# Kernel tuning notes

Hardware: AMD Instinct MI355X
Metric: run time of the kernel (lower is better)

## Reference

```python
import jax, jax.numpy as jnp
import numpy as np


def setup_inputs() -> dict:
    key = jax.random.key(0)
    k1, k2 = jax.random.split(key)
    inputs = jax.random.normal(k1, (64, 32, 32, 64), dtype=jnp.float32)
    # codebook param: (embedding_dim=64, n_embedding=1024), variance-scaling uniform fan_in
    fan_in = 64
    limit = float(np.sqrt(3.0 / fan_in))
    embeddings = jax.random.uniform(k2, (64, 1024), dtype=jnp.float32,
                                    minval=-limit, maxval=limit)
    return {"inputs": inputs, "embeddings": embeddings}


def reference(inputs, embeddings):
    commitment_cost = 0.25
    D, K = embeddings.shape  # (embedding_dim, n_embedding)
    flat = inputs.reshape(-1, D)  # [N, D]
    distances = (jnp.sum(jnp.square(flat), 1, keepdims=True)
                 - 2.0 * jnp.matmul(flat, embeddings)
                 + jnp.sum(jnp.square(embeddings), 0, keepdims=True))
    encoding_indices_flat = jnp.argmax(-distances, 1)  # [N]
    encodings = jax.nn.one_hot(encoding_indices_flat, K, dtype=distances.dtype)  # [N, K]
    encoding_indices = encoding_indices_flat.reshape(inputs.shape[:-1])  # [B,H,W]
    quantized = embeddings.T[encoding_indices]  # gather -> [B,H,W,D]

    e_latent_loss = jnp.mean(jnp.square(jax.lax.stop_gradient(quantized) - inputs))
    q_latent_loss = jnp.mean(jnp.square(quantized - jax.lax.stop_gradient(inputs)))
    loss = q_latent_loss + commitment_cost * e_latent_loss

    # straight-through estimator
    quantized_st = inputs + jax.lax.stop_gradient(quantized - inputs)

    avg_probs = jnp.mean(encodings, 0)
    perplexity = jnp.exp(-jnp.sum(avg_probs * jnp.log(avg_probs + 1e-10)))
    return (quantized_st, loss, perplexity, encodings, encoding_indices, distances)
```

## Files before the change

kernel.cpp:

```cpp
#include <hip/hip_runtime.h>
#include <math.h>

#define NROWS   65536
#define DIMS    64
#define KCODES  1024

static constexpr size_t QST_OFF  = 0;
static constexpr size_t LOSS_OFF = 4194304;
static constexpr size_t PERP_OFF = 4194305;
static constexpr size_t ENC_OFF  = 4194306;
static constexpr size_t IDX_OFF  = 71303170;
static constexpr size_t DIST_OFF = 71368706;

#define XSTRIDE 132

__global__ void enorm_kernel(const float* __restrict__ emb, float* __restrict__ enorm) {
    #pragma clang fp contract(off)
    int k = blockIdx.x * blockDim.x + threadIdx.x;
    float s = 0.f;
    for (int d = 0; d < DIMS; ++d) {
        float e  = emb[(size_t)d * KCODES + k];
        float sq = e * e;
        s = s + sq;
    }
    enorm[k] = s;
}

__global__ __launch_bounds__(512, 4) void vq_dist(
    const float* __restrict__ x, const float* __restrict__ emb,
    const float* __restrict__ enorm, float* __restrict__ out,
    unsigned long long* __restrict__ winners)
{
    #pragma clang fp contract(off)
    __shared__ __align__(16) float xs_t[32 * XSTRIDE];
    __shared__ __align__(16) float es_t[32 * XSTRIDE];
    __shared__ float xnl[128];

    const int tid = threadIdx.x;
    const int tc  = tid & 15;
    const int tr  = tid >> 4;
    const int kt  = blockIdx.x & 7;
    const int br  = blockIdx.x >> 3;
    const size_t n0 = (size_t)br * 128;

    const float* xg = x + n0 * DIMS;
    const float* eg = emb + kt * 128;

    float acc[4][8];
    #pragma unroll
    for (int j = 0; j < 4; ++j)
        #pragma unroll
        for (int jj = 0; jj < 8; ++jj) acc[j][jj] = 0.f;

    float rr[8];

    for (int h = 0; h < 2; ++h) {
        __syncthreads();
        #pragma unroll
        for (int i = 0; i < 2; ++i) {
            int c = tid + 512 * i;
            int row = c >> 3, dq = c & 7;
            float4 v = *(const float4*)(xg + (size_t)row * DIMS + h * 32 + dq * 4);
            xs_t[(dq * 4 + 0) * XSTRIDE + row] = v.x;
            xs_t[(dq * 4 + 1) * XSTRIDE + row] = v.y;
            xs_t[(dq * 4 + 2) * XSTRIDE + row] = v.z;
            xs_t[(dq * 4 + 3) * XSTRIDE + row] = v.w;
        }
        #pragma unroll
        for (int i = 0; i < 2; ++i) {
            int c = tid + 512 * i;
            int d2 = c >> 5, kq = c & 31;
            float4 v = *(const float4*)(eg + (size_t)(h * 32 + d2) * KCODES + kq * 4);
            es_t[d2 * XSTRIDE + kq * 4 + 0] = v.x;
            es_t[d2 * XSTRIDE + kq * 4 + 1] = v.y;
            es_t[d2 * XSTRIDE + kq * 4 + 2] = v.z;
            es_t[d2 * XSTRIDE + kq * 4 + 3] = v.w;
        }
        __syncthreads();

        if (tid < 128) {
            if (h == 0) {
                #pragma unroll
                for (int j = 0; j < 8; ++j) { float v = xs_t[j * XSTRIDE + tid]; rr[j] = v * v; }
                for (int i = 8; i < 32; i += 8)
                    #pragma unroll
                    for (int j = 0; j < 8; ++j) { float v = xs_t[(i + j) * XSTRIDE + tid]; float sq = v * v; rr[j] = rr[j] + sq; }
            } else {
                for (int i = 0; i < 32; i += 8)
                    #pragma unroll
                    for (int j = 0; j < 8; ++j) { float v = xs_t[(i + j) * XSTRIDE + tid]; float sq = v * v; rr[j] = rr[j] + sq; }
                xnl[tid] = ((rr[0] + rr[1]) + (rr[2] + rr[3])) + ((rr[4] + rr[5]) + (rr[6] + rr[7]));
            }
        }

        #pragma unroll 4
        for (int d2 = 0; d2 < 32; ++d2) {
            float4 xr = *(const float4*)&xs_t[d2 * XSTRIDE + tr * 4];
            float4 ea = *(const float4*)&es_t[d2 * XSTRIDE + tc * 4];
            float4 eb = *(const float4*)&es_t[d2 * XSTRIDE + 64 + tc * 4];
            float xv[4] = {xr.x, xr.y, xr.z, xr.w};
            #pragma unroll
            for (int j = 0; j < 4; ++j) {
                acc[j][0] = fmaf(xv[j], ea.x, acc[j][0]);
                acc[j][1] = fmaf(xv[j], ea.y, acc[j][1]);
                acc[j][2] = fmaf(xv[j], ea.z, acc[j][2]);
                acc[j][3] = fmaf(xv[j], ea.w, acc[j][3]);
                acc[j][4] = fmaf(xv[j], eb.x, acc[j][4]);
                acc[j][5] = fmaf(xv[j], eb.y, acc[j][5]);
                acc[j][6] = fmaf(xv[j], eb.z, acc[j][6]);
                acc[j][7] = fmaf(xv[j], eb.w, acc[j][7]);
            }
        }
    }
    __syncthreads();

    const float4 en0 = *(const float4*)(enorm + kt * 128 + tc * 4);
    const float4 en1 = *(const float4*)(enorm + kt * 128 + 64 + tc * 4);
    const float4 z4 = make_float4(0.f, 0.f, 0.f, 0.f);

    #pragma unroll
    for (int j = 0; j < 4; ++j) {
        const int row = tr * 4 + j;
        const float xnr = xnl[row];
        float4 da, db;
        { float m = 2.0f * acc[j][0]; float t = xnr - m; da.x = t + en0.x; }
        { float m = 2.0f * acc[j][1]; float t = xnr - m; da.y = t + en0.y; }
        { float m = 2.0f * acc[j][2]; float t = xnr - m; da.z = t + en0.z; }
        { float m = 2.0f * acc[j][3]; float t = xnr - m; da.w = t + en0.w; }
        { float m = 2.0f * acc[j][4]; float t = xnr - m; db.x = t + en1.x; }
        { float m = 2.0f * acc[j][5]; float t = xnr - m; db.y = t + en1.y; }
        { float m = 2.0f * acc[j][6]; float t = xnr - m; db.z = t + en1.z; }
        { float m = 2.0f * acc[j][7]; float t = xnr - m; db.w = t + en1.w; }

        const size_t rowg = n0 + row;
        float* dr = out + DIST_OFF + rowg * (size_t)KCODES + kt * 128 + tc * 4;
        *(float4*)dr = da; *(float4*)(dr + 64) = db;
        float* er = out + ENC_OFF + rowg * (size_t)KCODES + kt * 128 + tc * 4;
        *(float4*)er = z4; *(float4*)(er + 64) = z4;

        float bv = da.x; int kloc = tc * 4;
        if (da.y < bv) { bv = da.y; kloc = tc * 4 + 1; }
        if (da.z < bv) { bv = da.z; kloc = tc * 4 + 2; }
        if (da.w < bv) { bv = da.w; kloc = tc * 4 + 3; }
        if (db.x < bv) { bv = db.x; kloc = 64 + tc * 4; }
        if (db.y < bv) { bv = db.y; kloc = 64 + tc * 4 + 1; }
        if (db.z < bv) { bv = db.z; kloc = 64 + tc * 4 + 2; }
        if (db.w < bv) { bv = db.w; kloc = 64 + tc * 4 + 3; }

        int ib = __float_as_int(bv);
        unsigned mk = (unsigned)ib ^ ((unsigned)(ib >> 31) | 0x80000000u);
        unsigned long long key = ((unsigned long long)mk << 32) | (unsigned)(kt * 128 + kloc);

        #pragma unroll
        for (int m = 1; m < 16; m <<= 1) {
            unsigned long long ok = __shfl_xor(key, m);
            if (ok < key) key = ok;
        }
        if (tc == 0) atomicMin(&winners[rowg], key);
    }
}

__global__ __launch_bounds__(256) void vq_finish(
    const float* __restrict__ x, const float* __restrict__ emb,
    const unsigned long long* __restrict__ winners, float* __restrict__ out,
    float* __restrict__ counts, float* __restrict__ sqsum)
{
    __shared__ float bsum[4];
    const int tid = threadIdx.x;
    const size_t row = (size_t)blockIdx.x * 16 + (tid >> 4);
    const int q = tid & 15;
    const int k = (int)(winners[row] & 1023u);

    float4 e4;
    e4.x = emb[(size_t)(q * 4 + 0) * KCODES + k];
    e4.y = emb[(size_t)(q * 4 + 1) * KCODES + k];
    e4.z = emb[(size_t)(q * 4 + 2) * KCODES + k];
    e4.w = emb[(size_t)(q * 4 + 3) * KCODES + k];
    float4 x4 = *(const float4*)(x + row * DIMS + q * 4);
    *(float4*)(out + QST_OFF + row * DIMS + q * 4) = e4;

    float f0 = e4.x - x4.x, f1 = e4.y - x4.y, f2 = e4.z - x4.z, f3 = e4.w - x4.w;
    float ls = f0 * f0 + f1 * f1 + f2 * f2 + f3 * f3;
    #pragma unroll
    for (int m = 1; m < 64; m <<= 1) ls += __shfl_xor(ls, m);
    if ((tid & 63) == 0) bsum[tid >> 6] = ls;

    if (q == 0) {
        out[IDX_OFF + row] = (float)k;
        atomicAdd(&counts[k], 1.0f);
        out[ENC_OFF + row * (size_t)KCODES + k] = 1.0f;
    }
    __syncthreads();
    if (tid == 0) atomicAdd(sqsum, (bsum[0] + bsum[1]) + (bsum[2] + bsum[3]));
}

__global__ void vq_final(const float* __restrict__ counts, const float* __restrict__ sqsum,
                         float* __restrict__ out) {
    __shared__ double part[16];
    int tid = threadIdx.x;
    double p = (double)counts[tid] * (1.0 / 65536.0);
    double t = p * log(p + 1e-10);
    #pragma unroll
    for (int m = 1; m < 64; m <<= 1) t += __shfl_xor(t, m);
    if ((tid & 63) == 0) part[tid >> 6] = t;
    __syncthreads();
    if (tid == 0) {
        double s = 0.0;
        #pragma unroll
        for (int i = 0; i < 16; ++i) s += part[i];
        out[LOSS_OFF] = (float)(1.25 * (double)sqsum[0] * (1.0 / 4194304.0));
        out[PERP_OFF] = (float)exp(-s);
    }
}

extern "C" void kernel_launch(void* const* d_in, const int* in_sizes, int n_in,
                              void* d_out, int out_size, void* d_ws, size_t ws_size,
                              hipStream_t stream) {
    const float* x   = (const float*)d_in[0];
    const float* emb = (const float*)d_in[1];
    float* out = (float*)d_out;
    float* enorm  = (float*)d_ws;
    float* counts = enorm + KCODES;
    float* sqsum  = counts + KCODES;
    unsigned long long* winners = (unsigned long long*)((float*)d_ws + 4096);

    hipMemsetAsync(counts, 0, (KCODES + 1) * sizeof(float), stream);
    hipMemsetAsync(winners, 0xFF, NROWS * sizeof(unsigned long long), stream);
    enorm_kernel<<<KCODES / 256, 256, 0, stream>>>(emb, enorm);
    vq_dist<<<(NROWS / 128) * (KCODES / 128), 512, 0, stream>>>(x, emb, enorm, out, winners);
    vq_finish<<<NROWS / 16, 256, 0, stream>>>(x, emb, winners, out, counts, sqsum);
    vq_final<<<1, KCODES, 0, stream>>>(counts, sqsum, out);
}
```

Measured before the change: 264.8 us.

## Fuse distance, argmin and finish into one row-block kernel with double-buffered codebook

Each block now handles 128 rows against all 1024 codes, looping over code tiles with double-buffered shared-memory codebook slices and prefetching. The per-row argmin is kept in registers, which removes the global winners buffer, its memset and the 64-bit atomicMin. The quantized gather and loss are done in the same kernel using a transposed codebook built in the prep kernel. The trade-off is a much smaller grid and larger shared-memory footprint, which lowers parallelism for the store-heavy output writes.

```diff
diff --git a/kernel.cpp b/kernel.cpp
--- a/kernel.cpp
+++ b/kernel.cpp
@@ -4,6 +4,7 @@
 #define NROWS   65536
 #define DIMS    64
 #define KCODES  1024
+#define XL      132
 
 static constexpr size_t QST_OFF  = 0;
 static constexpr size_t LOSS_OFF = 4194304;
@@ -12,92 +13,98 @@
 static constexpr size_t IDX_OFF  = 71303170;
 static constexpr size_t DIST_OFF = 71368706;
 
-#define XSTRIDE 132
-
-__global__ void enorm_kernel(const float* __restrict__ emb, float* __restrict__ enorm) {
+__global__ void prep_kernel(const float* __restrict__ emb, float* __restrict__ enorm,
+                            float* __restrict__ embT) {
     #pragma clang fp contract(off)
     int k = blockIdx.x * blockDim.x + threadIdx.x;
     float s = 0.f;
     for (int d = 0; d < DIMS; ++d) {
-        float e  = emb[(size_t)d * KCODES + k];
+        float e = emb[(size_t)d * KCODES + k];
+        embT[(size_t)k * DIMS + d] = e;
         float sq = e * e;
         s = s + sq;
     }
     enorm[k] = s;
 }
 
-__global__ __launch_bounds__(512, 4) void vq_dist(
+__global__ __launch_bounds__(512, 4) void vq_fused(
     const float* __restrict__ x, const float* __restrict__ emb,
-    const float* __restrict__ enorm, float* __restrict__ out,
-    unsigned long long* __restrict__ winners)
+    const float* __restrict__ enorm, const float* __restrict__ embT,
+    float* __restrict__ out, float* __restrict__ counts, float* __restrict__ sqsum)
 {
     #pragma clang fp contract(off)
-    __shared__ __align__(16) float xs_t[32 * XSTRIDE];
-    __shared__ __align__(16) float es_t[32 * XSTRIDE];
-    __shared__ float xnl[128];
+    __shared__ __align__(16) float xs[DIMS * XL];
+    __shared__ __align__(16) float es[2][32 * XL];
+    __shared__ float xn[128];
+    __shared__ int   winner[128];
+    __shared__ float bsum[8];
 
     const int tid = threadIdx.x;
     const int tc  = tid & 15;
     const int tr  = tid >> 4;
-    const int kt  = blockIdx.x & 7;
-    const int br  = blockIdx.x >> 3;
-    const size_t n0 = (size_t)br * 128;
-
+    const size_t n0 = (size_t)blockIdx.x * 128;
     const float* xg = x + n0 * DIMS;
-    const float* eg = emb + kt * 128;
+
+    #pragma unroll
+    for (int i = 0; i < 4; ++i) {
+        int c = tid + 512 * i;
+        int row = c & 127, dq = c >> 7;
+        float4 v = *(const float4*)(xg + (size_t)row * DIMS + dq * 4);
+        xs[(dq * 4 + 0) * XL + row] = v.x;
+        xs[(dq * 4 + 1) * XL + row] = v.y;
+        xs[(dq * 4 + 2) * XL + row] = v.z;
+        xs[(dq * 4 + 3) * XL + row] = v.w;
+    }
+    {
+        int c0 = tid, c1 = tid + 512;
+        float4 a = *(const float4*)(emb + (size_t)(c0 >> 5) * KCODES + (c0 & 31) * 4);
+        float4 b = *(const float4*)(emb + (size_t)(c1 >> 5) * KCODES + (c1 & 31) * 4);
+        __syncthreads();
+        *(float4*)&es[0][(c0 >> 5) * XL + (c0 & 31) * 4] = a;
+        *(float4*)&es[0][(c1 >> 5) * XL + (c1 & 31) * 4] = b;
+    }
+    if (tid < 128) {
+        float rr[8];
+        #pragma unroll
+        for (int j = 0; j < 8; ++j) { float v = xs[j * XL + tid]; rr[j] = v * v; }
+        for (int i = 8; i < 64; i += 8)
+            #pragma unroll
+            for (int j = 0; j < 8; ++j) { float v = xs[(i + j) * XL + tid]; float sq = v * v; rr[j] = rr[j] + sq; }
+        xn[tid] = ((rr[0] + rr[1]) + (rr[2] + rr[3])) + ((rr[4] + rr[5]) + (rr[6] + rr[7]));
+    }
+    __syncthreads();
 
     float acc[4][8];
-    #pragma unroll
-    for (int j = 0; j < 4; ++j)
-        #pragma unroll
-        for (int jj = 0; jj < 8; ++jj) acc[j][jj] = 0.f;
-
-    float rr[8];
-
-    for (int h = 0; h < 2; ++h) {
-        __syncthreads();
-        #pragma unroll
-        for (int i = 0; i < 2; ++i) {
-            int c = tid + 512 * i;
-            int row = c >> 3, dq = c & 7;
-            float4 v = *(const float4*)(xg + (size_t)row * DIMS + h * 32 + dq * 4);
-            xs_t[(dq * 4 + 0) * XSTRIDE + row] = v.x;
-            xs_t[(dq * 4 + 1) * XSTRIDE + row] = v.y;
-            xs_t[(dq * 4 + 2) * XSTRIDE + row] = v.z;
-            xs_t[(dq * 4 + 3) * XSTRIDE + row] = v.w;
-        }
-        #pragma unroll
-        for (int i = 0; i < 2; ++i) {
-            int c = tid + 512 * i;
-            int d2 = c >> 5, kq = c & 31;
-            float4 v = *(const float4*)(eg + (size_t)(h * 32 + d2) * KCODES + kq * 4);
-            es_t[d2 * XSTRIDE + kq * 4 + 0] = v.x;
-            es_t[d2 * XSTRIDE + kq * 4 + 1] = v.y;
-            es_t[d2 * XSTRIDE + kq * 4 + 2] = v.z;
-            es_t[d2 * XSTRIDE + kq * 4 + 3] = v.w;
-        }
-        __syncthreads();
-
-        if (tid < 128) {
-            if (h == 0) {
+    float bv[4]; int bi[4];
+    #pragma unroll
+    for (int j = 0; j < 4; ++j) { bv[j] = 3.4e38f; bi[j] = 0; }
+    float4 en0, en1;
+    const float4 z4 = make_float4(0.f, 0.f, 0.f, 0.f);
+
+    for (int s = 0; s < 16; ++s) {
+        const int kt = s >> 1, h = s & 1, buf = s & 1;
+        if (h == 0) {
+            #pragma unroll
+            for (int j = 0; j < 4; ++j)
                 #pragma unroll
-                for (int j = 0; j < 8; ++j) { float v = xs_t[j * XSTRIDE + tid]; rr[j] = v * v; }
-                for (int i = 8; i < 32; i += 8)
-                    #pragma unroll
-                    for (int j = 0; j < 8; ++j) { float v = xs_t[(i + j) * XSTRIDE + tid]; float sq = v * v; rr[j] = rr[j] + sq; }
-            } else {
-                for (int i = 0; i < 32; i += 8)
-                    #pragma unroll
-                    for (int j = 0; j < 8; ++j) { float v = xs_t[(i + j) * XSTRIDE + tid]; float sq = v * v; rr[j] = rr[j] + sq; }
-                xnl[tid] = ((rr[0] + rr[1]) + (rr[2] + rr[3])) + ((rr[4] + rr[5]) + (rr[6] + rr[7]));
-            }
-        }
-
+                for (int m = 0; m < 8; ++m) acc[j][m] = 0.f;
+            en0 = *(const float4*)(enorm + kt * 128 + tc * 4);
+            en1 = *(const float4*)(enorm + kt * 128 + 64 + tc * 4);
+        }
+        float4 nt0, nt1;
+        if (s < 15) {
+            int sn = s + 1, ktn = sn >> 1, hn = sn & 1;
+            int c0 = tid, c1 = tid + 512;
+            nt0 = *(const float4*)(emb + (size_t)(hn * 32 + (c0 >> 5)) * KCODES + ktn * 128 + (c0 & 31) * 4);
+            nt1 = *(const float4*)(emb + (size_t)(hn * 32 + (c1 >> 5)) * KCODES + ktn * 128 + (c1 & 31) * 4);
+        }
+        const float* ep = es[buf];
+        const int dbase = h * 32;
         #pragma unroll 4
         for (int d2 = 0; d2 < 32; ++d2) {
-            float4 xr = *(const float4*)&xs_t[d2 * XSTRIDE + tr * 4];
-            float4 ea = *(const float4*)&es_t[d2 * XSTRIDE + tc * 4];
-            float4 eb = *(const float4*)&es_t[d2 * XSTRIDE + 64 + tc * 4];
+            float4 xr = *(const float4*)&xs[(dbase + d2) * XL + tr * 4];
+            float4 ea = *(const float4*)&ep[d2 * XL + tc * 4];
+            float4 eb = *(const float4*)&ep[d2 * XL + 64 + tc * 4];
             float xv[4] = {xr.x, xr.y, xr.z, xr.w};
             #pragma unroll
             for (int j = 0; j < 4; ++j) {
@@ -111,87 +118,98 @@
                 acc[j][7] = fmaf(xv[j], eb.w, acc[j][7]);
             }
         }
-    }
-    __syncthreads();
-
-    const float4 en0 = *(const float4*)(enorm + kt * 128 + tc * 4);
-    const float4 en1 = *(const float4*)(enorm + kt * 128 + 64 + tc * 4);
-    const float4 z4 = make_float4(0.f, 0.f, 0.f, 0.f);
+        if (h == 1) {
+            #pragma unroll
+            for (int j = 0; j < 4; ++j) {
+                const int row = tr * 4 + j;
+                const float xnr = xn[row];
+                float4 da, db;
+                { float m = 2.0f * acc[j][0]; float t = xnr - m; da.x = t + en0.x; }
+                { float m = 2.0f * acc[j][1]; float t = xnr - m; da.y = t + en0.y; }
+                { float m = 2.0f * acc[j][2]; float t = xnr - m; da.z = t + en0.z; }
+                { float m = 2.0f * acc[j][3]; float t = xnr - m; da.w = t + en0.w; }
+                { float m = 2.0f * acc[j][4]; float t = xnr - m; db.x = t + en1.x; }
+                { float m = 2.0f * acc[j][5]; float t = xnr - m; db.y = t + en1.y; }
+                { float m = 2.0f * acc[j][6]; float t = xnr - m; db.z = t + en1.z; }
+                { float m = 2.0f * acc[j][7]; float t = xnr - m; db.w = t + en1.w; }
+                const size_t rowg = n0 + row;
+                float* dr = out + DIST_OFF + rowg * (size_t)KCODES + kt * 128 + tc * 4;
+                *(float4*)dr = da; *(float4*)(dr + 64) = db;
+                float* er = out + ENC_OFF + rowg * (size_t)KCODES + kt * 128 + tc * 4;
+                *(float4*)er = z4; *(float4*)(er + 64) = z4;
+
+                float lv = da.x; int li = kt * 128 + tc * 4;
+                if (da.y < lv) { lv = da.y; li = kt * 128 + tc * 4 + 1; }
+                if (da.z < lv) { lv = da.z; li = kt * 128 + tc * 4 + 2; }
+                if (da.w < lv) { lv = da.w; li = kt * 128 + tc * 4 + 3; }
+                if (db.x < lv) { lv = db.x; li = kt * 128 + 64 + tc * 4; }
+                if (db.y < lv) { lv = db.y; li = kt * 128 + 64 + tc * 4 + 1; }
+                if (db.z < lv) { lv = db.z; li = kt * 128 + 64 + tc * 4 + 2; }
+                if (db.w < lv) { lv = db.w; li = kt * 128 + 64 + tc * 4 + 3; }
+                if (lv < bv[j]) { bv[j] = lv; bi[j] = li; }
+            }
+        }
+        if (s < 15) {
+            int bufn = (s + 1) & 1;
+            int c0 = tid, c1 = tid + 512;
+            *(float4*)&es[bufn][(c0 >> 5) * XL + (c0 & 31) * 4] = nt0;
+            *(float4*)&es[bufn][(c1 >> 5) * XL + (c1 & 31) * 4] = nt1;
+        }
+        asm volatile("s_waitcnt lgkmcnt(0)" ::: "memory");
+        __builtin_amdgcn_s_barrier();
+    }
+
+    __syncthreads();
 
     #pragma unroll
     for (int j = 0; j < 4; ++j) {
         const int row = tr * 4 + j;
-        const float xnr = xnl[row];
-        float4 da, db;
-        { float m = 2.0f * acc[j][0]; float t = xnr - m; da.x = t + en0.x; }
-        { float m = 2.0f * acc[j][1]; float t = xnr - m; da.y = t + en0.y; }
-        { float m = 2.0f * acc[j][2]; float t = xnr - m; da.z = t + en0.z; }
-        { float m = 2.0f * acc[j][3]; float t = xnr - m; da.w = t + en0.w; }
-        { float m = 2.0f * acc[j][4]; float t = xnr - m; db.x = t + en1.x; }
-        { float m = 2.0f * acc[j][5]; float t = xnr - m; db.y = t + en1.y; }
-        { float m = 2.0f * acc[j][6]; float t = xnr - m; db.z = t + en1.z; }
-        { float m = 2.0f * acc[j][7]; float t = xnr - m; db.w = t + en1.w; }
-
-        const size_t rowg = n0 + row;
-        float* dr = out + DIST_OFF + rowg * (size_t)KCODES + kt * 128 + tc * 4;
-        *(float4*)dr = da; *(float4*)(dr + 64) = db;
-        float* er = out + ENC_OFF + rowg * (size_t)KCODES + kt * 128 + tc * 4;
-        *(float4*)er = z4; *(float4*)(er + 64) = z4;
-
-        float bv = da.x; int kloc = tc * 4;
-        if (da.y < bv) { bv = da.y; kloc = tc * 4 + 1; }
-        if (da.z < bv) { bv = da.z; kloc = tc * 4 + 2; }
-        if (da.w < bv) { bv = da.w; kloc = tc * 4 + 3; }
-        if (db.x < bv) { bv = db.x; kloc = 64 + tc * 4; }
-        if (db.y < bv) { bv = db.y; kloc = 64 + tc * 4 + 1; }
-        if (db.z < bv) { bv = db.z; kloc = 64 + tc * 4 + 2; }
-        if (db.w < bv) { bv = db.w; kloc = 64 + tc * 4 + 3; }
-
-        int ib = __float_as_int(bv);
+        int ib = __float_as_int(bv[j]);
         unsigned mk = (unsigned)ib ^ ((unsigned)(ib >> 31) | 0x80000000u);
-        unsigned long long key = ((unsigned long long)mk << 32) | (unsigned)(kt * 128 + kloc);
-
+        unsigned long long key = ((unsigned long long)mk << 32) | (unsigned)bi[j];
         #pragma unroll
         for (int m = 1; m < 16; m <<= 1) {
             unsigned long long ok = __shfl_xor(key, m);
             if (ok < key) key = ok;
         }
-        if (tc == 0) atomicMin(&winners[rowg], key);
-    }
-}
-
-__global__ __launch_bounds__(256) void vq_finish(
-    const float* __restrict__ x, const float* __restrict__ emb,
-    const unsigned long long* __restrict__ winners, float* __restrict__ out,
-    float* __restrict__ counts, float* __restrict__ sqsum)
-{
-    __shared__ float bsum[4];
-    const int tid = threadIdx.x;
-    const size_t row = (size_t)blockIdx.x * 16 + (tid >> 4);
-    const int q = tid & 15;
-    const int k = (int)(winners[row] & 1023u);
-
-    float4 e4;
-    e4.x = emb[(size_t)(q * 4 + 0) * KCODES + k];
-    e4.y = emb[(size_t)(q * 4 + 1) * KCODES + k];
-    e4.z = emb[(size_t)(q * 4 + 2) * KCODES + k];
-    e4.w = emb[(size_t)(q * 4 + 3) * KCODES + k];
-    float4 x4 = *(const float4*)(x + row * DIMS + q * 4);
-    *(float4*)(out + QST_OFF + row * DIMS + q * 4) = e4;
-
-    float f0 = e4.x - x4.x, f1 = e4.y - x4.y, f2 = e4.z - x4.z, f3 = e4.w - x4.w;
-    float ls = f0 * f0 + f1 * f1 + f2 * f2 + f3 * f3;
-    #pragma unroll
-    for (int m = 1; m < 64; m <<= 1) ls += __shfl_xor(ls, m);
-    if ((tid & 63) == 0) bsum[tid >> 6] = ls;
-
-    if (q == 0) {
-        out[IDX_OFF + row] = (float)k;
-        atomicAdd(&counts[k], 1.0f);
-        out[ENC_OFF + row * (size_t)KCODES + k] = 1.0f;
-    }
-    __syncthreads();
-    if (tid == 0) atomicAdd(sqsum, (bsum[0] + bsum[1]) + (bsum[2] + bsum[3]));
+        if (tc == 0) {
+            int k = (int)(key & 1023u);
+            winner[row] = k;
+            out[IDX_OFF + n0 + row] = (float)k;
+            atomicAdd(&counts[k], 1.0f);
+            out[ENC_OFF + (n0 + row) * (size_t)KCODES + k] = 1.0f;
+        }
+    }
+    __syncthreads();
+
+    {
+        const int row = tid >> 2;
+        const int q4  = tid & 3;
+        const int k   = winner[row];
+        const float* et = embT + (size_t)k * DIMS + q4 * 16;
+        float* qo = out + QST_OFF + (n0 + row) * (size_t)DIMS + q4 * 16;
+        float ls = 0.f;
+        #pragma unroll
+        for (int i = 0; i < 4; ++i) {
+            float4 q = *(const float4*)(et + 4 * i);
+            *(float4*)(qo + 4 * i) = q;
+            float f0 = q.x - xs[(q4 * 16 + 4 * i + 0) * XL + row];
+            float f1 = q.y - xs[(q4 * 16 + 4 * i + 1) * XL + row];
+            float f2 = q.z - xs[(q4 * 16 + 4 * i + 2) * XL + row];
+            float f3 = q.w - xs[(q4 * 16 + 4 * i + 3) * XL + row];
+            ls += f0 * f0 + f1 * f1 + f2 * f2 + f3 * f3;
+        }
+        #pragma unroll
+        for (int m = 1; m < 64; m <<= 1) ls += __shfl_xor(ls, m);
+        if ((tid & 63) == 0) bsum[tid >> 6] = ls;
+    }
+    __syncthreads();
+    if (tid == 0) {
+        float s = 0.f;
+        #pragma unroll
+        for (int i = 0; i < 8; ++i) s += bsum[i];
+        atomicAdd(sqsum, s);
+    }
 }
 
 __global__ void vq_final(const float* __restrict__ counts, const float* __restrict__ sqsum,
@@ -222,12 +240,10 @@
     float* enorm  = (float*)d_ws;
     float* counts = enorm + KCODES;
     float* sqsum  = counts + KCODES;
-    unsigned long long* winners = (unsigned long long*)((float*)d_ws + 4096);
+    float* embT   = (float*)d_ws + 4096;
 
     hipMemsetAsync(counts, 0, (KCODES + 1) * sizeof(float), stream);
-    hipMemsetAsync(winners, 0xFF, NROWS * sizeof(unsigned long long), stream);
-    enorm_kernel<<<KCODES / 256, 256, 0, stream>>>(emb, enorm);
-    vq_dist<<<(NROWS / 128) * (KCODES / 128), 512, 0, stream>>>(x, emb, enorm, out, winners);
-    vq_finish<<<NROWS / 16, 256, 0, stream>>>(x, emb, winners, out, counts, sqsum);
+    prep_kernel<<<KCODES / 256, 256, 0, stream>>>(emb, enorm, embT);
+    vq_fused<<<NROWS / 128, 512, 0, stream>>>(x, emb, enorm, embT, out, counts, sqsum);
     vq_final<<<1, KCODES, 0, stream>>>(counts, sqsum, out);
 }
```

Result: no change. 266.6 us (+0.7%).

## Restructure distance kernel: load x tile once, loop over codebook tiles, nontemporal stores

Applied to the files above, without the earlier changes.

Each block of the distance kernel now loads its 128-row x tile into shared memory once and loops over four 128-code tiles, covering half the codebook. Previously eight blocks each reloaded the same x rows. Each thread computes an 8x8 output tile, reading embeddings straight from global memory with register prefetch instead of staging them in LDS. It keeps a running per-row argmin across tiles, so only one shuffle reduction and atomic happens per row. Distance, one-hot and quantized outputs use nontemporal 8-byte or 16-byte stores to limit cache pollution. In exchange, higher register pressure (64 accumulators) lowers occupancy, and the global stores are narrower than before.

```diff
diff --git a/kernel.cpp b/kernel.cpp
--- a/kernel.cpp
+++ b/kernel.cpp
@@ -4,6 +4,10 @@
 #define NROWS   65536
 #define DIMS    64
 #define KCODES  1024
+#define XL      132
+
+typedef float f32x2 __attribute__((ext_vector_type(2)));
+typedef float f32x4 __attribute__((ext_vector_type(4)));
 
 static constexpr size_t QST_OFF  = 0;
 static constexpr size_t LOSS_OFF = 4194304;
@@ -11,8 +15,6 @@
 static constexpr size_t ENC_OFF  = 4194306;
 static constexpr size_t IDX_OFF  = 71303170;
 static constexpr size_t DIST_OFF = 71368706;
-
-#define XSTRIDE 132
 
 __global__ void enorm_kernel(const float* __restrict__ emb, float* __restrict__ enorm) {
     #pragma clang fp contract(off)
@@ -26,137 +28,133 @@
     enorm[k] = s;
 }
 
-__global__ __launch_bounds__(512, 4) void vq_dist(
+__global__ __launch_bounds__(256, 3) void vq_dist(
     const float* __restrict__ x, const float* __restrict__ emb,
     const float* __restrict__ enorm, float* __restrict__ out,
     unsigned long long* __restrict__ winners)
 {
     #pragma clang fp contract(off)
-    __shared__ __align__(16) float xs_t[32 * XSTRIDE];
-    __shared__ __align__(16) float es_t[32 * XSTRIDE];
-    __shared__ float xnl[128];
+    __shared__ __align__(16) float xs[DIMS * XL];
+    __shared__ float xn[128];
 
     const int tid = threadIdx.x;
     const int tc  = tid & 15;
     const int tr  = tid >> 4;
-    const int kt  = blockIdx.x & 7;
-    const int br  = blockIdx.x >> 3;
-    const size_t n0 = (size_t)br * 128;
-
+    const int kb  = blockIdx.x & 1;
+    const int rb  = blockIdx.x >> 1;
+    const size_t n0 = (size_t)rb * 128;
     const float* xg = x + n0 * DIMS;
-    const float* eg = emb + kt * 128;
-
-    float acc[4][8];
-    #pragma unroll
-    for (int j = 0; j < 4; ++j)
-        #pragma unroll
-        for (int jj = 0; jj < 8; ++jj) acc[j][jj] = 0.f;
-
-    float rr[8];
-
-    for (int h = 0; h < 2; ++h) {
-        __syncthreads();
-        #pragma unroll
-        for (int i = 0; i < 2; ++i) {
-            int c = tid + 512 * i;
-            int row = c >> 3, dq = c & 7;
-            float4 v = *(const float4*)(xg + (size_t)row * DIMS + h * 32 + dq * 4);
-            xs_t[(dq * 4 + 0) * XSTRIDE + row] = v.x;
-            xs_t[(dq * 4 + 1) * XSTRIDE + row] = v.y;
-            xs_t[(dq * 4 + 2) * XSTRIDE + row] = v.z;
-            xs_t[(dq * 4 + 3) * XSTRIDE + row] = v.w;
+
+    #pragma unroll
+    for (int i = 0; i < 8; ++i) {
+        int c = i * 256 + tid;
+        int row = c >> 4, q = c & 15;
+        float4 v = *(const float4*)(xg + (size_t)row * DIMS + q * 4);
+        xs[(q * 4 + 0) * XL + row] = v.x;
+        xs[(q * 4 + 1) * XL + row] = v.y;
+        xs[(q * 4 + 2) * XL + row] = v.z;
+        xs[(q * 4 + 3) * XL + row] = v.w;
+    }
+    __syncthreads();
+    if (tid < 128) {
+        float rr[8];
+        #pragma unroll
+        for (int j = 0; j < 8; ++j) { float v = xs[j * XL + tid]; rr[j] = v * v; }
+        for (int i = 8; i < 64; i += 8)
+            #pragma unroll
+            for (int j = 0; j < 8; ++j) { float v = xs[(i + j) * XL + tid]; float sq = v * v; rr[j] = rr[j] + sq; }
+        xn[tid] = ((rr[0] + rr[1]) + (rr[2] + rr[3])) + ((rr[4] + rr[5]) + (rr[6] + rr[7]));
+    }
+    __syncthreads();
+
+    float bv[8]; int bi[8];
+    #pragma unroll
+    for (int j = 0; j < 8; ++j) { bv[j] = 3.4e38f; bi[j] = 0; }
+
+    for (int kt = 0; kt < 4; ++kt) {
+        const int kbase = kb * 512 + kt * 128 + tc * 8;
+        float acc[8][8];
+        #pragma unroll
+        for (int j = 0; j < 8; ++j)
+            #pragma unroll
+            for (int m = 0; m < 8; ++m) acc[j][m] = 0.f;
+
+        const float* ebase = emb + kbase;
+        float4 eA = *(const float4*)(ebase);
+        float4 eB = *(const float4*)(ebase + 4);
+        #pragma unroll 4
+        for (int d = 0; d < DIMS; ++d) {
+            float4 eAn, eBn;
+            if (d < DIMS - 1) {
+                const float* ep = ebase + (size_t)(d + 1) * KCODES;
+                eAn = *(const float4*)(ep);
+                eBn = *(const float4*)(ep + 4);
+            }
+            float4 x0 = *(const float4*)&xs[d * XL + tr * 8];
+            float4 x1 = *(const float4*)&xs[d * XL + tr * 8 + 4];
+            const float xv[8] = {x0.x, x0.y, x0.z, x0.w, x1.x, x1.y, x1.z, x1.w};
+            #pragma unroll
+            for (int j = 0; j < 8; ++j) {
+                acc[j][0] = fmaf(xv[j], eA.x, acc[j][0]);
+                acc[j][1] = fmaf(xv[j], eA.y, acc[j][1]);
+                acc[j][2] = fmaf(xv[j], eA.z, acc[j][2]);
+                acc[j][3] = fmaf(xv[j], eA.w, acc[j][3]);
+                acc[j][4] = fmaf(xv[j], eB.x, acc[j][4]);
+                acc[j][5] = fmaf(xv[j], eB.y, acc[j][5]);
+                acc[j][6] = fmaf(xv[j], eB.z, acc[j][6]);
+                acc[j][7] = fmaf(xv[j], eB.w, acc[j][7]);
+            }
+            eA = eAn; eB = eBn;
         }
-        #pragma unroll
-        for (int i = 0; i < 2; ++i) {
-            int c = tid + 512 * i;
-            int d2 = c >> 5, kq = c & 31;
-            float4 v = *(const float4*)(eg + (size_t)(h * 32 + d2) * KCODES + kq * 4);
-            es_t[d2 * XSTRIDE + kq * 4 + 0] = v.x;
-            es_t[d2 * XSTRIDE + kq * 4 + 1] = v.y;
-            es_t[d2 * XSTRIDE + kq * 4 + 2] = v.z;
-            es_t[d2 * XSTRIDE + kq * 4 + 3] = v.w;
+
+        const float4 enA = *(const float4*)(enorm + kbase);
+        const float4 enB = *(const float4*)(enorm + kbase + 4);
+        const float en[8] = {enA.x, enA.y, enA.z, enA.w, enB.x, enB.y, enB.z, enB.w};
+
+        #pragma unroll
+        for (int j = 0; j < 8; ++j) {
+            const int row = tr * 8 + j;
+            const float xnr = xn[row];
+            float dv[8];
+            #pragma unroll
+            for (int m = 0; m < 8; ++m) {
+                float mm = 2.0f * acc[j][m];
+                float tt = xnr - mm;
+                dv[m] = tt + en[m];
+            }
+            const size_t rowg = n0 + row;
+            float* dr = out + DIST_OFF + rowg * (size_t)KCODES + kbase;
+            f32x2 v01 = {dv[0], dv[1]}, v23 = {dv[2], dv[3]};
+            f32x2 v45 = {dv[4], dv[5]}, v67 = {dv[6], dv[7]};
+            __builtin_nontemporal_store(v01, (f32x2*)(dr));
+            __builtin_nontemporal_store(v23, (f32x2*)(dr + 2));
+            __builtin_nontemporal_store(v45, (f32x2*)(dr + 4));
+            __builtin_nontemporal_store(v67, (f32x2*)(dr + 6));
+            float* er = out + ENC_OFF + rowg * (size_t)KCODES + kbase;
+            const f32x2 z2 = {0.f, 0.f};
+            __builtin_nontemporal_store(z2, (f32x2*)(er));
+            __builtin_nontemporal_store(z2, (f32x2*)(er + 2));
+            __builtin_nontemporal_store(z2, (f32x2*)(er + 4));
+            __builtin_nontemporal_store(z2, (f32x2*)(er + 6));
+
+            float lv = dv[0]; int li = kbase;
+            #pragma unroll
+            for (int m = 1; m < 8; ++m) if (dv[m] < lv) { lv = dv[m]; li = kbase + m; }
+            if (lv < bv[j]) { bv[j] = lv; bi[j] = li; }
         }
-        __syncthreads();
-
-        if (tid < 128) {
-            if (h == 0) {
-                #pragma unroll
-                for (int j = 0; j < 8; ++j) { float v = xs_t[j * XSTRIDE + tid]; rr[j] = v * v; }
-                for (int i = 8; i < 32; i += 8)
-                    #pragma unroll
-                    for (int j = 0; j < 8; ++j) { float v = xs_t[(i + j) * XSTRIDE + tid]; float sq = v * v; rr[j] = rr[j] + sq; }
-            } else {
-                for (int i = 0; i < 32; i += 8)
-                    #pragma unroll
-                    for (int j = 0; j < 8; ++j) { float v = xs_t[(i + j) * XSTRIDE + tid]; float sq = v * v; rr[j] = rr[j] + sq; }
-                xnl[tid] = ((rr[0] + rr[1]) + (rr[2] + rr[3])) + ((rr[4] + rr[5]) + (rr[6] + rr[7]));
-            }
-        }
-
-        #pragma unroll 4
-        for (int d2 = 0; d2 < 32; ++d2) {
-            float4 xr = *(const float4*)&xs_t[d2 * XSTRIDE + tr * 4];
-            float4 ea = *(const float4*)&es_t[d2 * XSTRIDE + tc * 4];
-            float4 eb = *(const float4*)&es_t[d2 * XSTRIDE + 64 + tc * 4];
-            float xv[4] = {xr.x, xr.y, xr.z, xr.w};
-            #pragma unroll
-            for (int j = 0; j < 4; ++j) {
-                acc[j][0] = fmaf(xv[j], ea.x, acc[j][0]);
-                acc[j][1] = fmaf(xv[j], ea.y, acc[j][1]);
-                acc[j][2] = fmaf(xv[j], ea.z, acc[j][2]);
-                acc[j][3] = fmaf(xv[j], ea.w, acc[j][3]);
-                acc[j][4] = fmaf(xv[j], eb.x, acc[j][4]);
-                acc[j][5] = fmaf(xv[j], eb.y, acc[j][5]);
-                acc[j][6] = fmaf(xv[j], eb.z, acc[j][6]);
-                acc[j][7] = fmaf(xv[j], eb.w, acc[j][7]);
-            }
-        }
-    }
-    __syncthreads();
-
-    const float4 en0 = *(const float4*)(enorm + kt * 128 + tc * 4);
-    const float4 en1 = *(const float4*)(enorm + kt * 128 + 64 + tc * 4);
-    const float4 z4 = make_float4(0.f, 0.f, 0.f, 0.f);
-
-    #pragma unroll
-    for (int j = 0; j < 4; ++j) {
-        const int row = tr * 4 + j;
-        const float xnr = xnl[row];
-        float4 da, db;
-        { float m = 2.0f * acc[j][0]; float t = xnr - m; da.x = t + en0.x; }
-        { float m = 2.0f * acc[j][1]; float t = xnr - m; da.y = t + en0.y; }
-        { float m = 2.0f * acc[j][2]; float t = xnr - m; da.z = t + en0.z; }
-        { float m = 2.0f * acc[j][3]; float t = xnr - m; da.w = t + en0.w; }
-        { float m = 2.0f * acc[j][4]; float t = xnr - m; db.x = t + en1.x; }
-        { float m = 2.0f * acc[j][5]; float t = xnr - m; db.y = t + en1.y; }
-        { float m = 2.0f * acc[j][6]; float t = xnr - m; db.z = t + en1.z; }
-        { float m = 2.0f * acc[j][7]; float t = xnr - m; db.w = t + en1.w; }
-
-        const size_t rowg = n0 + row;
-        float* dr = out + DIST_OFF + rowg * (size_t)KCODES + kt * 128 + tc * 4;
-        *(float4*)dr = da; *(float4*)(dr + 64) = db;
-        float* er = out + ENC_OFF + rowg * (size_t)KCODES + kt * 128 + tc * 4;
-        *(float4*)er = z4; *(float4*)(er + 64) = z4;
-
-        float bv = da.x; int kloc = tc * 4;
-        if (da.y < bv) { bv = da.y; kloc = tc * 4 + 1; }
-        if (da.z < bv) { bv = da.z; kloc = tc * 4 + 2; }
-        if (da.w < bv) { bv = da.w; kloc = tc * 4 + 3; }
-        if (db.x < bv) { bv = db.x; kloc = 64 + tc * 4; }
-        if (db.y < bv) { bv = db.y; kloc = 64 + tc * 4 + 1; }
-        if (db.z < bv) { bv = db.z; kloc = 64 + tc * 4 + 2; }
-        if (db.w < bv) { bv = db.w; kloc = 64 + tc * 4 + 3; }
-
-        int ib = __float_as_int(bv);
+    }
+
+    #pragma unroll
+    for (int j = 0; j < 8; ++j) {
+        int ib = __float_as_int(bv[j]);
         unsigned mk = (unsigned)ib ^ ((unsigned)(ib >> 31) | 0x80000000u);
-        unsigned long long key = ((unsigned long long)mk << 32) | (unsigned)(kt * 128 + kloc);
-
+        unsigned long long key = ((unsigned long long)mk << 32) | (unsigned)bi[j];
         #pragma unroll
         for (int m = 1; m < 16; m <<= 1) {
             unsigned long long ok = __shfl_xor(key, m);
             if (ok < key) key = ok;
         }
-        if (tc == 0) atomicMin(&winners[rowg], key);
+        if (tc == 0) atomicMin(&winners[n0 + tr * 8 + j], key);
     }
 }
 
@@ -171,13 +169,13 @@
     const int q = tid & 15;
     const int k = (int)(winners[row] & 1023u);
 
-    float4 e4;
+    f32x4 e4;
     e4.x = emb[(size_t)(q * 4 + 0) * KCODES + k];
     e4.y = emb[(size_t)(q * 4 + 1) * KCODES + k];
     e4.z = emb[(size_t)(q * 4 + 2) * KCODES + k];
     e4.w = emb[(size_t)(q * 4 + 3) * KCODES + k];
     float4 x4 = *(const float4*)(x + row * DIMS + q * 4);
-    *(float4*)(out + QST_OFF + row * DIMS + q * 4) = e4;
+    __builtin_nontemporal_store(e4, (f32x4*)(out + QST_OFF + row * DIMS + q * 4));
 
     float f0 = e4.x - x4.x, f1 = e4.y - x4.y, f2 = e4.z - x4.z, f3 = e4.w - x4.w;
     float ls = f0 * f0 + f1 * f1 + f2 * f2 + f3 * f3;
@@ -227,7 +225,7 @@
     hipMemsetAsync(counts, 0, (KCODES + 1) * sizeof(float), stream);
     hipMemsetAsync(winners, 0xFF, NROWS * sizeof(unsigned long long), stream);
     enorm_kernel<<<KCODES / 256, 256, 0, stream>>>(emb, enorm);
-    vq_dist<<<(NROWS / 128) * (KCODES / 128), 512, 0, stream>>>(x, emb, enorm, out, winners);
+    vq_dist<<<(NROWS / 128) * 2, 256, 0, stream>>>(x, emb, enorm, out, winners);
     vq_finish<<<NROWS / 16, 256, 0, stream>>>(x, emb, winners, out, counts, sqsum);
     vq_final<<<1, KCODES, 0, stream>>>(counts, sqsum, out);
 }
```

Result: slower. 409.8 us (+54.8%).
